# Kernel tuning notes

Hardware: AMD Instinct MI355X
Metric: run time of the kernel (lower is better)

## Reference

```python
import jax, jax.numpy as jnp
import numpy as np

HIDDEN = 1024
NUM_HEADS = 16
HEAD_DIM = HIDDEN // NUM_HEADS
BLOCK_SIZE = 2048
LN_EPS = 1e-12


def layer_norm(x, g, b, eps=LN_EPS):
    mu = jnp.mean(x, axis=-1, keepdims=True)
    var = jnp.mean(jnp.square(x - mu), axis=-1, keepdims=True)
    return (x - mu) * jax.lax.rsqrt(var + eps) * g + b


def setup_inputs() -> dict:
    key = jax.random.key(0)
    ks = jax.random.split(key, 10)
    B, S_CTX, S_Q = 4, 8192, 2048
    scale = 1.0 / np.sqrt(HIDDEN)
    inp = {
        "input_ids": jax.random.normal(ks[0], (B, S_CTX, HIDDEN), jnp.float32),
        "query_input": jax.random.normal(ks[1], (B, S_Q, HIDDEN), jnp.float32),
        "Wq": jax.random.normal(ks[2], (HIDDEN, HIDDEN), jnp.float32) * scale,
        "bq": jnp.zeros((HIDDEN,), jnp.float32),
        "Wk": jax.random.normal(ks[3], (HIDDEN, HIDDEN), jnp.float32) * scale,
        "bk": jnp.zeros((HIDDEN,), jnp.float32),
        "Wv": jax.random.normal(ks[4], (HIDDEN, HIDDEN), jnp.float32) * scale,
        "bv": jnp.zeros((HIDDEN,), jnp.float32),
        "ln_g": jnp.ones((HIDDEN,), jnp.float32),
        "ln_b": jnp.zeros((HIDDEN,), jnp.float32),
        "host_id": 2,
    }
    return inp


def reference(input_ids, query_input, Wq, bq, Wk, bk, Wv, bv, ln_g, ln_b, host_id):
    B = input_ids.shape[0]
    start = host_id * BLOCK_SIZE  # host_id is a static Python int
    # Phase 1: local context encoding (anchor_key is computed in the original
    # but never used downstream, so it does not affect the output)
    local_block = input_ids[:, start:start + BLOCK_SIZE]          # (B, Skv, H)
    local_h = layer_norm(local_block, ln_g, ln_b)
    k = (local_h @ Wk + bk).reshape(B, BLOCK_SIZE, NUM_HEADS, HEAD_DIM)
    v = (local_h @ Wv + bv).reshape(B, BLOCK_SIZE, NUM_HEADS, HEAD_DIM)
    # Phase 2: query encoding; dropout is identity (p=0 / eval mode)
    Sq = query_input.shape[1]
    q_h = layer_norm(query_input, ln_g, ln_b)
    q = (q_h @ Wq + bq).reshape(B, Sq, NUM_HEADS, HEAD_DIM)
    scores = jnp.einsum("bqhd,bkhd->bhqk", q, k) / np.sqrt(HEAD_DIM)
    probs = jax.nn.softmax(scores, axis=-1)                       # (B, H, Sq, Skv)
    ctx = jnp.einsum("bhqk,bkhd->bqhd", probs, v)
    return ctx.reshape(B, Sq, HIDDEN)
```

## Files before the change

kernel.cpp:

```cpp
#include <hip/hip_runtime.h>

#define B_    4
#define SCTX  8192
#define SQ    2048
#define SK    2048
#define HID   1024
#define NH    16
#define HD    64
#define MQ    (B_*SQ)
#define MK    (B_*SK)

typedef float f32x4  __attribute__((ext_vector_type(4)));
typedef short bf16x8 __attribute__((ext_vector_type(8)));

__device__ __forceinline__ unsigned short f2b(float f) {
    union { float f; unsigned u; } v; v.f = f;
    unsigned r = v.u + 0x7FFFu + ((v.u >> 16) & 1u);
    return (unsigned short)(r >> 16);
}

__device__ __forceinline__ int decode_host_id(const unsigned* p) {
    unsigned w0 = p[0];
    int hid;
    if (w0 > 0u && w0 < 8u) hid = (int)w0;
    else if (w0 == 0u) {
        unsigned w1 = p[1];
        hid = (w1 == 0u) ? 0 : (int)__hiloint2double((int)w1, 0);
    } else hid = (int)__uint_as_float(w0);
    if (hid < 0) hid = 0;
    if (hid > SCTX/SK - 1) hid = SCTX/SK - 1;
    return hid;
}

__device__ __forceinline__ void gload16(const unsigned short* g, unsigned short* l) {
    __builtin_amdgcn_global_load_lds(
        (const __attribute__((address_space(1))) void*)g,
        (__attribute__((address_space(3))) void*)l, 16, 0, 0);
}

__global__ void ln_kernel(const float* __restrict__ query,
                          const float* __restrict__ input_ids,
                          const unsigned* __restrict__ host_id,
                          const float* __restrict__ g,
                          const float* __restrict__ lb,
                          unsigned short* __restrict__ hq,
                          unsigned short* __restrict__ hk) {
    int row = blockIdx.x;
    int start = decode_host_id(host_id) * SK;
    const float* src;
    unsigned short* dst;
    if (row < MQ) {
        src = query + (size_t)row * HID;
        dst = hq + (size_t)row * HID;
    } else {
        int r = row - MQ;
        int b = r >> 11, s = r & 2047;
        src = input_ids + ((size_t)b * SCTX + start + s) * HID;
        dst = hk + (size_t)r * HID;
    }
    int t = threadIdx.x;
    float4 x = ((const float4*)src)[t];
    float s1 = x.x + x.y + x.z + x.w;
    float s2 = x.x*x.x + x.y*x.y + x.z*x.z + x.w*x.w;
    for (int off = 32; off > 0; off >>= 1) {
        s1 += __shfl_xor(s1, off, 64);
        s2 += __shfl_xor(s2, off, 64);
    }
    __shared__ float red[8];
    int w = t >> 6;
    if ((t & 63) == 0) { red[w*2] = s1; red[w*2+1] = s2; }
    __syncthreads();
    s1 = red[0] + red[2] + red[4] + red[6];
    s2 = red[1] + red[3] + red[5] + red[7];
    float mu   = s1 * (1.0f / HID);
    float var  = s2 * (1.0f / HID) - mu * mu;
    float rstd = rsqrtf(fmaxf(var, 0.0f) + 1e-12f);
    float4 gv = ((const float4*)g)[t];
    float4 bv = ((const float4*)lb)[t];
    ushort4 o;
    o.x = f2b((x.x - mu) * rstd * gv.x + bv.x);
    o.y = f2b((x.y - mu) * rstd * gv.y + bv.y);
    o.z = f2b((x.z - mu) * rstd * gv.z + bv.z);
    o.w = f2b((x.w - mu) * rstd * gv.w + bv.w);
    ((ushort4*)dst)[t] = o;
}

__global__ void transpose_kernel(const float* __restrict__ Wq,
                                 const float* __restrict__ Wk,
                                 const float* __restrict__ Wv,
                                 unsigned short* __restrict__ Wtq,
                                 unsigned short* __restrict__ Wtk,
                                 unsigned short* __restrict__ Wtv) {
    __shared__ unsigned short tile[64][66];
    int z = blockIdx.z;
    const float* src = (z == 0) ? Wq : (z == 1) ? Wk : Wv;
    unsigned short* dst = (z == 0) ? Wtq : (z == 1) ? Wtk : Wtv;
    int tx = threadIdx.x & 63;
    int ty = threadIdx.x >> 6;
    int k0 = blockIdx.x * 64;
    int n0 = blockIdx.y * 64;
    for (int i = ty; i < 64; i += 4)
        tile[i][tx] = f2b(src[(size_t)(k0 + i) * HID + n0 + tx]);
    __syncthreads();
    for (int i = ty; i < 64; i += 4)
        dst[(size_t)(n0 + i) * HID + k0 + tx] = tile[tx][i];
}

#define BM 128
#define BN 128
#define BKg 32

__global__ __launch_bounds__(256, 3) void gemm3_kernel(
        const unsigned short* __restrict__ hq,
        const unsigned short* __restrict__ hk,
        const unsigned short* __restrict__ Wtq,
        const unsigned short* __restrict__ Wtk,
        const unsigned short* __restrict__ Wtv,
        const float* __restrict__ bq,
        const float* __restrict__ bk,
        const float* __restrict__ bv,
        unsigned short* __restrict__ Qb,
        unsigned short* __restrict__ Kb,
        unsigned short* __restrict__ Vtb) {
    __shared__ __align__(16) unsigned short As[2][BM * BKg];
    __shared__ __align__(16) unsigned short Bs[2][BN * BKg];

    int z = blockIdx.z;
    const unsigned short* A  = (z == 0) ? hq : hk;
    const unsigned short* Bt = (z == 0) ? Wtq : (z == 1) ? Wtk : Wtv;
    const float* bias        = (z == 0) ? bq  : (z == 1) ? bk  : bv;
    unsigned short* out      = (z == 0) ? Qb  : (z == 1) ? Kb  : Vtb;
    float scale = (z == 0) ? 0.18033688f : 1.0f;
    int epi = (z == 2);

    int t = threadIdx.x;
    int lane = t & 63;
    int w = t >> 6;
    int wr = w >> 1, wc = w & 1;
    int qd = lane >> 4, c = lane & 15;

    int bid = (int)(blockIdx.y * gridDim.x + blockIdx.x);
    int xcd = bid & 7, kk = bid >> 3;
    int bx = xcd * 8 + (kk & 7);
    int by = kk >> 3;
    size_t m0 = (size_t)bx * BM;
    size_t n0 = (size_t)by * BN;

    int s0 = t, s1 = t + 256;
    int ar0 = s0 >> 2, ac0 = (s0 & 3) * 8;
    int ar1 = s1 >> 2, ac1 = (s1 & 3) * 8;

#define STAGE(buf, kk0) do { \
    gload16(A  + (m0 + ar0) * HID + (kk0) + ac0, &As[buf][s0 * 8]); \
    gload16(A  + (m0 + ar1) * HID + (kk0) + ac1, &As[buf][s1 * 8]); \
    gload16(Bt + (n0 + ar0) * HID + (kk0) + ac0, &Bs[buf][s0 * 8]); \
    gload16(Bt + (n0 + ar1) * HID + (kk0) + ac1, &Bs[buf][s1 * 8]); \
} while (0)

    f32x4 acc[4][4] = {};
    STAGE(0, 0);
    __syncthreads();
    int cur = 0;
    #pragma unroll 2
    for (int kt = 0; kt < HID/BKg; kt++) {
        if (kt + 1 < HID/BKg) STAGE(cur ^ 1, (kt + 1) * BKg);
        bf16x8 a[4], b[4];
        #pragma unroll
        for (int mi = 0; mi < 4; mi++)
            a[mi] = *(const bf16x8*)(&As[cur][(wr*64 + mi*16 + c) * BKg + qd*8]);
        #pragma unroll
        for (int ni = 0; ni < 4; ni++)
            b[ni] = *(const bf16x8*)(&Bs[cur][(wc*64 + ni*16 + c) * BKg + qd*8]);
        #pragma unroll
        for (int mi = 0; mi < 4; mi++)
            #pragma unroll
            for (int ni = 0; ni < 4; ni++)
                acc[mi][ni] = __builtin_amdgcn_mfma_f32_16x16x32_bf16(a[mi], b[ni], acc[mi][ni], 0, 0, 0);
        __syncthreads();
        cur ^= 1;
    }
#undef STAGE

    #pragma unroll
    for (int ni = 0; ni < 4; ni++) {
        int n = (int)n0 + wc*64 + ni*16 + c;
        float bn = bias[n];
        #pragma unroll
        for (int mi = 0; mi < 4; mi++) {
            int mbase = (int)m0 + wr*64 + mi*16 + qd*4;
            if (epi == 0) {
                #pragma unroll
                for (int r = 0; r < 4; r++)
                    out[(size_t)(mbase + r) * HID + n] = f2b((acc[mi][ni][r] + bn) * scale);
            } else {
                int bb = mbase >> 11, s = mbase & 2047;
                int h = n >> 6, d = n & 63;
                ushort4 pk;
                pk.x = f2b(acc[mi][ni][0] + bn);
                pk.y = f2b(acc[mi][ni][1] + bn);
                pk.z = f2b(acc[mi][ni][2] + bn);
                pk.w = f2b(acc[mi][ni][3] + bn);
                *(ushort4*)(out + (((size_t)(bb*NH + h))*HD + d)*SK + s) = pk;
            }
        }
    }
}

__global__ __launch_bounds__(64) void attn_kernel(
        const unsigned short* __restrict__ Q,
        const unsigned short* __restrict__ K,
        const unsigned short* __restrict__ Vt,
        float* __restrict__ out) {
    __shared__ __align__(16) unsigned short P[64][72];
    int lane = threadIdx.x;
    int qd = lane >> 4, c = lane & 15;
    int q0 = blockIdx.x * 64;
    int h  = blockIdx.y;
    int b  = blockIdx.z;

    bf16x8 qf[4][2];
    #pragma unroll
    for (int mi = 0; mi < 4; mi++)
        #pragma unroll
        for (int ks = 0; ks < 2; ks++)
            qf[mi][ks] = *(const bf16x8*)(Q + ((size_t)(b*SQ + q0 + mi*16 + c))*HID + h*HD + ks*32 + qd*8);

    float lsum[4][4];
    f32x4 o[4][4] = {};
    #pragma unroll
    for (int mi = 0; mi < 4; mi++)
        #pragma unroll
        for (int r = 0; r < 4; r++) lsum[mi][r] = 0.0f;

    for (int kt = 0; kt < SK/64; kt++) {
        int key0 = kt * 64;
        bf16x8 kf[4][2];
        #pragma unroll
        for (int ni = 0; ni < 4; ni++)
            #pragma unroll
            for (int ks = 0; ks < 2; ks++)
                kf[ni][ks] = *(const bf16x8*)(K + ((size_t)(b*SK + key0 + ni*16 + c))*HID + h*HD + ks*32 + qd*8);
        f32x4 s[4][4] = {};
        #pragma unroll
        for (int mi = 0; mi < 4; mi++)
            #pragma unroll
            for (int ni = 0; ni < 4; ni++) {
                s[mi][ni] = __builtin_amdgcn_mfma_f32_16x16x32_bf16(qf[mi][0], kf[ni][0], s[mi][ni], 0, 0, 0);
                s[mi][ni] = __builtin_amdgcn_mfma_f32_16x16x32_bf16(qf[mi][1], kf[ni][1], s[mi][ni], 0, 0, 0);
            }
        bf16x8 vf[4][2];
        #pragma unroll
        for (int ni = 0; ni < 4; ni++)
            #pragma unroll
            for (int ks = 0; ks < 2; ks++)
                vf[ni][ks] = *(const bf16x8*)(Vt + (((size_t)(b*NH + h))*HD + ni*16 + c)*SK + key0 + ks*32 + qd*8);
        #pragma unroll
        for (int mi = 0; mi < 4; mi++) {
            #pragma unroll
            for (int ni = 0; ni < 4; ni++)
                #pragma unroll
                for (int r = 0; r < 4; r++) {
                    float p = exp2f(fminf(s[mi][ni][r], 50.0f));
                    s[mi][ni][r] = p;
                    lsum[mi][r] += p;
                }
            #pragma unroll
            for (int ni = 0; ni < 4; ni++)
                #pragma unroll
                for (int r = 0; r < 4; r++)
                    P[mi*16 + qd*4 + r][ni*16 + c] = f2b(s[mi][ni][r]);
        }
        asm volatile("s_waitcnt lgkmcnt(0)" ::: "memory");
        bf16x8 pf[4][2];
        #pragma unroll
        for (int mi = 0; mi < 4; mi++)
            #pragma unroll
            for (int ks = 0; ks < 2; ks++)
                pf[mi][ks] = *(const bf16x8*)(&P[mi*16 + c][ks*32 + qd*8]);
        #pragma unroll
        for (int mi = 0; mi < 4; mi++)
            #pragma unroll
            for (int ni = 0; ni < 4; ni++) {
                o[mi][ni] = __builtin_amdgcn_mfma_f32_16x16x32_bf16(pf[mi][0], vf[ni][0], o[mi][ni], 0, 0, 0);
                o[mi][ni] = __builtin_amdgcn_mfma_f32_16x16x32_bf16(pf[mi][1], vf[ni][1], o[mi][ni], 0, 0, 0);
            }
    }
    #pragma unroll
    for (int mi = 0; mi < 4; mi++)
        #pragma unroll
        for (int r = 0; r < 4; r++) {
            float l = lsum[mi][r];
            for (int off = 1; off < 16; off <<= 1) l += __shfl_xor(l, off, 16);
            lsum[mi][r] = 1.0f / l;
        }
    #pragma unroll
    for (int mi = 0; mi < 4; mi++)
        #pragma unroll
        for (int ni = 0; ni < 4; ni++)
            #pragma unroll
            for (int r = 0; r < 4; r++) {
                int m = q0 + mi*16 + qd*4 + r;
                out[((size_t)(b*SQ + m))*HID + h*HD + ni*16 + c] = o[mi][ni][r] * lsum[mi][r];
            }
}

extern "C" void kernel_launch(void* const* d_in, const int* in_sizes, int n_in,
                              void* d_out, int out_size, void* d_ws, size_t ws_size,
                              hipStream_t stream) {
    const float *input_ids = nullptr, *query = nullptr;
    const float *Ws[3] = {nullptr, nullptr, nullptr};
    const float *bs[5] = {nullptr, nullptr, nullptr, nullptr, nullptr};
    const unsigned *hostid = nullptr;
    int wi = 0, bi = 0;
    for (int i = 0; i < n_in; i++) {
        long sz = in_sizes[i];
        if      (sz == 33554432) input_ids = (const float*)d_in[i];
        else if (sz == 8388608)  query     = (const float*)d_in[i];
        else if (sz == 1048576)  { if (wi < 3) Ws[wi++] = (const float*)d_in[i]; }
        else if (sz == 1024)     { if (bi < 5) bs[bi++] = (const float*)d_in[i]; }
        else if (sz == 1 || sz == 2) hostid = (const unsigned*)d_in[i];
    }
    if (n_in != 11 || !input_ids || !query || wi != 3 || bi != 5 || !hostid) {
        input_ids = (const float*)d_in[0];  query = (const float*)d_in[1];
        Ws[0] = (const float*)d_in[2]; bs[0] = (const float*)d_in[3];
        Ws[1] = (const float*)d_in[4]; bs[1] = (const float*)d_in[5];
        Ws[2] = (const float*)d_in[6]; bs[2] = (const float*)d_in[7];
        bs[3] = (const float*)d_in[8]; bs[4] = (const float*)d_in[9];
        hostid = (const unsigned*)d_in[10];
    }
    const float *Wq = Ws[0], *Wk = Ws[1], *Wv = Ws[2];
    const float *bq = bs[0], *bk = bs[1], *bv = bs[2], *ln_g = bs[3], *ln_b = bs[4];
    float* out = (float*)d_out;

    char* ws = (char*)d_ws;
    unsigned short* hq  = (unsigned short*)ws; ws += (size_t)MQ * HID * 2;
    unsigned short* hk  = (unsigned short*)ws; ws += (size_t)MK * HID * 2;
    unsigned short* Wtq = (unsigned short*)ws; ws += (size_t)HID * HID * 2;
    unsigned short* Wtk = (unsigned short*)ws; ws += (size_t)HID * HID * 2;
    unsigned short* Wtv = (unsigned short*)ws; ws += (size_t)HID * HID * 2;
    unsigned short* Qb  = (unsigned short*)ws; ws += (size_t)MQ * HID * 2;
    unsigned short* Kb  = (unsigned short*)ws; ws += (size_t)MK * HID * 2;
    unsigned short* Vtb = (unsigned short*)ws; ws += (size_t)MK * HID * 2;

    ln_kernel<<<MQ + MK, 256, 0, stream>>>(query, input_ids, hostid, ln_g, ln_b, hq, hk);
    transpose_kernel<<<dim3(16, 16, 3), 256, 0, stream>>>(Wq, Wk, Wv, Wtq, Wtk, Wtv);
    gemm3_kernel<<<dim3(MQ/BM, HID/BN, 3), 256, 0, stream>>>(
        hq, hk, Wtq, Wtk, Wtv, bq, bk, bv, Qb, Kb, Vtb);
    attn_kernel<<<dim3(SQ/64, NH, B_), 64, 0, stream>>>(Qb, Kb, Vtb, out);
}
```

Measured before the change: 443.5 us.

## Merge LN and weight transpose launches, pipeline GEMM staging, use fast exp2

Combines the layer-norm and weight-transpose kernels into one launch, and has each LN block handle four rows with one wavefront per row and no shared-memory reduction. The projection GEMM main loop swaps __syncthreads for explicit vmcnt/lgkmcnt waits and raw barriers, so the next tile's global-to-LDS load can stay in flight while the current tile is computed. The attention softmax uses the hardware exp2 builtin instead of exp2f. The intent is to cut launch overhead, LN reduction cost and GEMM stall time. The vmcnt(4) count depends on exactly four outstanding loads per stage, which is fragile if the stage changes.

```diff
diff --git a/kernel.cpp b/kernel.cpp
--- a/kernel.cpp
+++ b/kernel.cpp
@@ -38,72 +38,82 @@
         (__attribute__((address_space(3))) void*)l, 16, 0, 0);
 }
 
-__global__ void ln_kernel(const float* __restrict__ query,
-                          const float* __restrict__ input_ids,
-                          const unsigned* __restrict__ host_id,
-                          const float* __restrict__ g,
-                          const float* __restrict__ lb,
-                          unsigned short* __restrict__ hq,
-                          unsigned short* __restrict__ hk) {
-    int row = blockIdx.x;
-    int start = decode_host_id(host_id) * SK;
-    const float* src;
-    unsigned short* dst;
-    if (row < MQ) {
-        src = query + (size_t)row * HID;
-        dst = hq + (size_t)row * HID;
+__global__ __launch_bounds__(256) void ln_tr_kernel(
+        const float* __restrict__ query,
+        const float* __restrict__ input_ids,
+        const unsigned* __restrict__ host_id,
+        const float* __restrict__ g,
+        const float* __restrict__ lb,
+        unsigned short* __restrict__ hq,
+        unsigned short* __restrict__ hk,
+        const float* __restrict__ Wq,
+        const float* __restrict__ Wk,
+        const float* __restrict__ Wv,
+        unsigned short* __restrict__ Wtq,
+        unsigned short* __restrict__ Wtk,
+        unsigned short* __restrict__ Wtv) {
+    __shared__ unsigned short tile[64][66];
+    int bid = blockIdx.x;
+    if (bid < 4096) {
+        int lane = threadIdx.x & 63;
+        int w = threadIdx.x >> 6;
+        int row = bid * 4 + w;
+        int start = decode_host_id(host_id) * SK;
+        const float* src;
+        unsigned short* dst;
+        if (row < MQ) {
+            src = query + (size_t)row * HID;
+            dst = hq + (size_t)row * HID;
+        } else {
+            int r = row - MQ;
+            int b = r >> 11, s = r & 2047;
+            src = input_ids + ((size_t)b * SCTX + start + s) * HID;
+            dst = hk + (size_t)r * HID;
+        }
+        float4 x[4];
+        #pragma unroll
+        for (int i = 0; i < 4; i++) x[i] = ((const float4*)src)[lane + i*64];
+        float s1 = 0.0f, s2 = 0.0f;
+        #pragma unroll
+        for (int i = 0; i < 4; i++) {
+            s1 += x[i].x + x[i].y + x[i].z + x[i].w;
+            s2 += x[i].x*x[i].x + x[i].y*x[i].y + x[i].z*x[i].z + x[i].w*x[i].w;
+        }
+        #pragma unroll
+        for (int off = 1; off < 64; off <<= 1) {
+            s1 += __shfl_xor(s1, off, 64);
+            s2 += __shfl_xor(s2, off, 64);
+        }
+        float mu   = s1 * (1.0f / HID);
+        float var  = s2 * (1.0f / HID) - mu * mu;
+        float rstd = rsqrtf(fmaxf(var, 0.0f) + 1e-12f);
+        #pragma unroll
+        for (int i = 0; i < 4; i++) {
+            float4 gv = ((const float4*)g)[lane + i*64];
+            float4 bv = ((const float4*)lb)[lane + i*64];
+            ushort4 o;
+            o.x = f2b((x[i].x - mu) * rstd * gv.x + bv.x);
+            o.y = f2b((x[i].y - mu) * rstd * gv.y + bv.y);
+            o.z = f2b((x[i].z - mu) * rstd * gv.z + bv.z);
+            o.w = f2b((x[i].w - mu) * rstd * gv.w + bv.w);
+            ((ushort4*)dst)[lane + i*64] = o;
+        }
     } else {
-        int r = row - MQ;
-        int b = r >> 11, s = r & 2047;
-        src = input_ids + ((size_t)b * SCTX + start + s) * HID;
-        dst = hk + (size_t)r * HID;
-    }
-    int t = threadIdx.x;
-    float4 x = ((const float4*)src)[t];
-    float s1 = x.x + x.y + x.z + x.w;
-    float s2 = x.x*x.x + x.y*x.y + x.z*x.z + x.w*x.w;
-    for (int off = 32; off > 0; off >>= 1) {
-        s1 += __shfl_xor(s1, off, 64);
-        s2 += __shfl_xor(s2, off, 64);
-    }
-    __shared__ float red[8];
-    int w = t >> 6;
-    if ((t & 63) == 0) { red[w*2] = s1; red[w*2+1] = s2; }
-    __syncthreads();
-    s1 = red[0] + red[2] + red[4] + red[6];
-    s2 = red[1] + red[3] + red[5] + red[7];
-    float mu   = s1 * (1.0f / HID);
-    float var  = s2 * (1.0f / HID) - mu * mu;
-    float rstd = rsqrtf(fmaxf(var, 0.0f) + 1e-12f);
-    float4 gv = ((const float4*)g)[t];
-    float4 bv = ((const float4*)lb)[t];
-    ushort4 o;
-    o.x = f2b((x.x - mu) * rstd * gv.x + bv.x);
-    o.y = f2b((x.y - mu) * rstd * gv.y + bv.y);
-    o.z = f2b((x.z - mu) * rstd * gv.z + bv.z);
-    o.w = f2b((x.w - mu) * rstd * gv.w + bv.w);
-    ((ushort4*)dst)[t] = o;
-}
-
-__global__ void transpose_kernel(const float* __restrict__ Wq,
-                                 const float* __restrict__ Wk,
-                                 const float* __restrict__ Wv,
-                                 unsigned short* __restrict__ Wtq,
-                                 unsigned short* __restrict__ Wtk,
-                                 unsigned short* __restrict__ Wtv) {
-    __shared__ unsigned short tile[64][66];
-    int z = blockIdx.z;
-    const float* src = (z == 0) ? Wq : (z == 1) ? Wk : Wv;
-    unsigned short* dst = (z == 0) ? Wtq : (z == 1) ? Wtk : Wtv;
-    int tx = threadIdx.x & 63;
-    int ty = threadIdx.x >> 6;
-    int k0 = blockIdx.x * 64;
-    int n0 = blockIdx.y * 64;
-    for (int i = ty; i < 64; i += 4)
-        tile[i][tx] = f2b(src[(size_t)(k0 + i) * HID + n0 + tx]);
-    __syncthreads();
-    for (int i = ty; i < 64; i += 4)
-        dst[(size_t)(n0 + i) * HID + k0 + tx] = tile[tx][i];
+        int id = bid - 4096;
+        int z = id >> 8;
+        int tid = id & 255;
+        const float* src = (z == 0) ? Wq : (z == 1) ? Wk : Wv;
+        unsigned short* dst = (z == 0) ? Wtq : (z == 1) ? Wtk : Wtv;
+        int tx = threadIdx.x & 63;
+        int ty = threadIdx.x >> 6;
+        int k0 = (tid & 15) * 64;
+        int n0 = (tid >> 4) * 64;
+        for (int i = ty; i < 64; i += 4)
+            tile[i][tx] = f2b(src[(size_t)(k0 + i) * HID + n0 + tx]);
+        __syncthreads();
+        for (int i = ty; i < 64; i += 4)
+            dst[(size_t)(n0 + i) * HID + k0 + tx] = tile[tx][i];
+    }
 }
 
 #define BM 128
@@ -157,29 +167,38 @@
     gload16(Bt + (n0 + ar1) * HID + (kk0) + ac1, &Bs[buf][s1 * 8]); \
 } while (0)
 
+#define COMPUTE(buf) do { \
+    bf16x8 a[4], b[4]; \
+    _Pragma("unroll") \
+    for (int mi = 0; mi < 4; mi++) \
+        a[mi] = *(const bf16x8*)(&As[buf][(wr*64 + mi*16 + c) * BKg + qd*8]); \
+    _Pragma("unroll") \
+    for (int ni = 0; ni < 4; ni++) \
+        b[ni] = *(const bf16x8*)(&Bs[buf][(wc*64 + ni*16 + c) * BKg + qd*8]); \
+    _Pragma("unroll") \
+    for (int mi = 0; mi < 4; mi++) \
+        _Pragma("unroll") \
+        for (int ni = 0; ni < 4; ni++) \
+            acc[mi][ni] = __builtin_amdgcn_mfma_f32_16x16x32_bf16(a[mi], b[ni], acc[mi][ni], 0, 0, 0); \
+} while (0)
+
     f32x4 acc[4][4] = {};
     STAGE(0, 0);
-    __syncthreads();
     int cur = 0;
-    #pragma unroll 2
-    for (int kt = 0; kt < HID/BKg; kt++) {
-        if (kt + 1 < HID/BKg) STAGE(cur ^ 1, (kt + 1) * BKg);
-        bf16x8 a[4], b[4];
-        #pragma unroll
-        for (int mi = 0; mi < 4; mi++)
-            a[mi] = *(const bf16x8*)(&As[cur][(wr*64 + mi*16 + c) * BKg + qd*8]);
-        #pragma unroll
-        for (int ni = 0; ni < 4; ni++)
-            b[ni] = *(const bf16x8*)(&Bs[cur][(wc*64 + ni*16 + c) * BKg + qd*8]);
-        #pragma unroll
-        for (int mi = 0; mi < 4; mi++)
-            #pragma unroll
-            for (int ni = 0; ni < 4; ni++)
-                acc[mi][ni] = __builtin_amdgcn_mfma_f32_16x16x32_bf16(a[mi], b[ni], acc[mi][ni], 0, 0, 0);
-        __syncthreads();
+    for (int kt = 0; kt < HID/BKg - 1; kt++) {
+        STAGE(cur ^ 1, (kt + 1) * BKg);
+        asm volatile("s_waitcnt vmcnt(4)" ::: "memory");
+        __builtin_amdgcn_s_barrier();
+        COMPUTE(cur);
+        asm volatile("s_waitcnt lgkmcnt(0)" ::: "memory");
+        __builtin_amdgcn_s_barrier();
         cur ^= 1;
     }
+    asm volatile("s_waitcnt vmcnt(0)" ::: "memory");
+    __builtin_amdgcn_s_barrier();
+    COMPUTE(cur);
 #undef STAGE
+#undef COMPUTE
 
     #pragma unroll
     for (int ni = 0; ni < 4; ni++) {
@@ -260,7 +279,7 @@
             for (int ni = 0; ni < 4; ni++)
                 #pragma unroll
                 for (int r = 0; r < 4; r++) {
-                    float p = exp2f(fminf(s[mi][ni][r], 50.0f));
+                    float p = __builtin_amdgcn_exp2f(fminf(s[mi][ni][r], 50.0f));
                     s[mi][ni][r] = p;
                     lsum[mi][r] += p;
                 }
@@ -342,8 +361,9 @@
     unsigned short* Kb  = (unsigned short*)ws; ws += (size_t)MK * HID * 2;
     unsigned short* Vtb = (unsigned short*)ws; ws += (size_t)MK * HID * 2;
 
-    ln_kernel<<<MQ + MK, 256, 0, stream>>>(query, input_ids, hostid, ln_g, ln_b, hq, hk);
-    transpose_kernel<<<dim3(16, 16, 3), 256, 0, stream>>>(Wq, Wk, Wv, Wtq, Wtk, Wtv);
+    ln_tr_kernel<<<4096 + 768, 256, 0, stream>>>(
+        query, input_ids, hostid, ln_g, ln_b, hq, hk,
+        Wq, Wk, Wv, Wtq, Wtk, Wtv);
     gemm3_kernel<<<dim3(MQ/BM, HID/BN, 3), 256, 0, stream>>>(
         hq, hk, Wtq, Wtk, Wtv, bq, bk, bv, Qb, Kb, Vtb);
     attn_kernel<<<dim3(SQ/64, NH, B_), 64, 0, stream>>>(Qb, Kb, Vtb, out);
```

Measured after the change: 418.2 us. -5.7%, faster.
